# Performance work log

Measured on AMD Instinct MI355X. Metric: run time of the kernel, lower is better.

The kernel has to match this reference:

```python
import jax, jax.numpy as jnp
import numpy as np

D, N, M = 256, 8192, 8192
DISTANCE_THRESH = 0.8


def setup_inputs() -> dict:
    key = jax.random.key(0)
    k0, k1 = jax.random.split(key)
    d0 = jax.random.normal(k0, (D, N), dtype=jnp.float32)
    d1 = jax.random.normal(k1, (D, M), dtype=jnp.float32)
    # descriptors are L2-normalized along the feature dim (cosine similarity,
    # consistent with the 2*(1-sim) squared-distance formula in the module)
    d0 = d0 / jnp.linalg.norm(d0, axis=0, keepdims=True)
    d1 = d1 / jnp.linalg.norm(d1, axis=0, keepdims=True)
    return {"descriptors0": d0, "descriptors1": d1}


def reference(descriptors0, descriptors1):
    # nn_sim: [N, M] similarity matrix
    nn_sim = jnp.einsum('dn,dm->nm', descriptors0, descriptors1)
    nn_dist_01 = jnp.max(nn_sim, axis=1)          # [N]
    nn_idx_01 = jnp.argmax(nn_sim, axis=1)        # [N]
    nn_idx_10 = jnp.argmax(nn_sim, axis=0)        # [M]
    nn_dist = 2.0 * (1.0 - nn_dist_01)            # squared L2 dist for unit vecs
    ids1 = jnp.arange(nn_sim.shape[0])
    mask = ids1 == nn_idx_10[nn_idx_01]           # mutual NN check
    if DISTANCE_THRESH > 0.0:
        mask = mask & (nn_dist <= DISTANCE_THRESH ** 2)
    matches = jnp.where(mask, nn_idx_01, -1)
    scores = jnp.where(mask, (nn_dist + 1.0) / 2.0, 0.0)
    return matches, scores
```

## Files before the change

kernel.cpp:

```cpp
#include <hip/hip_runtime.h>
#include <hip/hip_bf16.h>

typedef __attribute__((ext_vector_type(8))) short short8;
typedef __attribute__((ext_vector_type(4))) float floatx4;
typedef unsigned int u32;

#define D_DIM 256
#define TCOLS 32
#define TILES 8
#define IDX_BITS 0x1FFFu
#define VAL_MASK 0xFFFFE000u


__device__ inline unsigned short f2bf_rne(float f) {
  u32 u = __float_as_uint(f);
  u32 r = (u + 0x7FFFu + ((u >> 16) & 1u)) >> 16;
  return (unsigned short)r;
}

__device__ inline u32 umax(u32 a, u32 b) { return a > b ? a : b; }


__global__ __launch_bounds__(256) void transpose_cast2(const float* __restrict__ d0,
                                                       const float* __restrict__ d1,
                                                       unsigned short* __restrict__ At,
                                                       unsigned short* __restrict__ Bt2,
                                                       int N, int M,
                                                       u32* __restrict__ best, int init_n) {
  __shared__ alignas(16) unsigned short tile[64 * 132];
  const int tid = threadIdx.x;
  const int bx = blockIdx.x;
  const int nblkA = N / 64;
  const bool isA = bx < nblkA;
  const float* src = isA ? d0 : d1;
  const int C = isA ? N : M;
  const int gd0 = (isA ? bx : bx - nblkA) * 64;
  const int d = tid & 63;
  const int fy = blockIdx.y;
#pragma unroll
  for (int k = 0; k < 32; ++k) {
    int fl = (tid >> 6) + 4 * k;
    float v = src[(size_t)(fy * 128 + fl) * C + gd0 + d];
    tile[d * 132 + fl] = f2bf_rne(v);
  }
  __syncthreads();
  if (isA) {
#pragma unroll
    for (int c = 0; c < 4; ++c) {
      int slot = c * 256 + tid;
      int dd = slot >> 4, f8 = slot & 15;
      short8 o = *(const short8*)(tile + dd * 132 + f8 * 8);
      *(short8*)(At + (size_t)(gd0 + dd) * D_DIM + fy * 128 + f8 * 8) = o;
    }
  } else {
#pragma unroll
    for (int c = 0; c < 4; ++c) {
      int slot = c * 256 + tid;
      int dd = slot & 63;
      int f8l = c * 4 + (tid >> 6);
      int f8g = fy * 16 + f8l;
      short8 o = *(const short8*)(tile + dd * 132 + f8l * 8);
      size_t off = (size_t)((gd0 + dd) >> 5) * 8192 + (size_t)(f8g >> 2) * 1024 +
                   (size_t)((dd >> 4) & 1) * 512 + (f8g & 3) * 128 + (dd & 15) * 8;
      *(short8*)(Bt2 + off) = o;
    }
  }
  if (fy == 0) {
    int i = bx * 256 + tid;
    if (i < init_n) best[i] = 0u;
  }
}

template <bool PRECAST>
__global__ __launch_bounds__(256, 2) void gemm_reduce(const float* __restrict__ A,
                                                      const unsigned short* __restrict__ At,
                                                      const unsigned short* __restrict__ Bt2,
                                                      u32* __restrict__ best01,
                                                      u32* __restrict__ best10,
                                                      int N, int M) {
  __shared__ u32 colbest[TILES * TCOLS];

  const int tid  = threadIdx.x;
  const int wave = tid >> 6;
  const int lane = tid & 63;
  const int quad = lane >> 4;
  const int l15  = lane & 15;

  const int xB = N >> 8, yB = M >> 8;
  const int bid = blockIdx.x;
  int x, y;
  if ((yB & 7) == 0) {
    int c = bid & 7, k = bid >> 3;
    x = k % xB;
    y = c * (yB >> 3) + k / xB;
  } else {
    x = bid % xB;
    y = bid / xB;
  }
  const int n0  = x * 256;
  const int mg0 = y * (TILES * TCOLS);
  const int rbase = n0 + wave * 64;

  colbest[tid] = 0u;

  short8 af[4][8];
  if constexpr (PRECAST) {
#pragma unroll
    for (int t = 0; t < 4; ++t) {
      const unsigned short* ap = At + (size_t)(rbase + t * 16 + l15) * D_DIM + quad * 8;
#pragma unroll
      for (int kc = 0; kc < 8; ++kc)
        af[t][kc] = *(const short8*)(ap + kc * 32);
    }
  } else {
#pragma unroll
    for (int t = 0; t < 4; ++t)
#pragma unroll
      for (int kc = 0; kc < 8; ++kc) {
        const int row = rbase + t * 16 + l15;
        const int kb = kc * 32 + quad * 8;
        short8 o;
#pragma unroll
        for (int u = 0; u < 8; ++u)
          o[u] = (short)f2bf_rne(A[(size_t)(kb + u) * N + row]);
        af[t][kc] = o;
      }
  }

  const unsigned short* bp = Bt2 + (size_t)(mg0 >> 5) * 8192 + (size_t)lane * 8;

  short8 bfA[4][2];
#pragma unroll
  for (int kc = 0; kc < 4; ++kc)
#pragma unroll
    for (int j = 0; j < 2; ++j)
      bfA[kc][j] = *(const short8*)(bp + (kc * 2 + j) * 512);

  u32 rbk[16];
#pragma unroll
  for (int s = 0; s < 16; ++s) rbk[s] = 0u;
  const u32 rp0 = 0x1FFFu - (u32)(rbase + quad * 4);

  __syncthreads();

  for (int mt = 0; mt < TILES; ++mt) {
    const unsigned short* bpt = bp + (size_t)mt * 8192;
    floatx4 acc[4][2];
#pragma unroll
    for (int i = 0; i < 4; ++i)
#pragma unroll
      for (int j = 0; j < 2; ++j)
        acc[i][j] = (floatx4){2.0f, 2.0f, 2.0f, 2.0f};

#pragma unroll
    for (int kc = 0; kc < 4; ++kc)
#pragma unroll
      for (int i = 0; i < 4; ++i)
#pragma unroll
        for (int j = 0; j < 2; ++j)
          acc[i][j] = __builtin_amdgcn_mfma_f32_16x16x32_bf16(af[i][kc], bfA[kc][j], acc[i][j], 0, 0, 0);

#pragma unroll
    for (int kc = 0; kc < 4; ++kc)
#pragma unroll
      for (int j = 0; j < 2; ++j)
        bfA[kc][j] = *(const short8*)(bpt + ((kc + 4) * 2 + j) * 512);

#pragma unroll
    for (int kc = 0; kc < 4; ++kc)
#pragma unroll
      for (int i = 0; i < 4; ++i)
#pragma unroll
        for (int j = 0; j < 2; ++j)
          acc[i][j] = __builtin_amdgcn_mfma_f32_16x16x32_bf16(af[i][kc + 4], bfA[kc][j], acc[i][j], 0, 0, 0);

    if (mt + 1 < TILES) {
#pragma unroll
      for (int kc = 0; kc < 4; ++kc)
#pragma unroll
        for (int j = 0; j < 2; ++j)
          bfA[kc][j] = *(const short8*)(bpt + 8192 + (kc * 2 + j) * 512);
    }

    const int m0 = mg0 + mt * TCOLS;
    u32 cb[2] = {0u, 0u};
    u32 colpay[2] = {0x1FFFu - (u32)(m0 + l15), 0x1FFFu - (u32)(m0 + 16 + l15)};
#pragma unroll
    for (int i = 0; i < 4; ++i)
#pragma unroll
      for (int r = 0; r < 4; ++r) {
        u32 rp = rp0 - (u32)(i * 16 + r);
        u32 rb = rbk[i * 4 + r];
#pragma unroll
        for (int j = 0; j < 2; ++j) {
          u32 u = __float_as_uint(acc[i][j][r]) & VAL_MASK;
          rb = umax(rb, u | colpay[j]);
          cb[j] = umax(cb[j], u | rp);
        }
        rbk[i * 4 + r] = rb;
      }
#pragma unroll
    for (int j = 0; j < 2; ++j) {
      u32 b = cb[j];
      b = umax(b, (u32)__shfl_xor((int)b, 16, 64));
      b = umax(b, (u32)__shfl_xor((int)b, 32, 64));
      if (quad == 0) atomicMax(&colbest[mt * TCOLS + j * 16 + l15], b);
    }
  }

#pragma unroll
  for (int i = 0; i < 4; ++i)
#pragma unroll
    for (int r = 0; r < 4; ++r) {
      u32 b = rbk[i * 4 + r];
      b = umax(b, (u32)__shfl_xor((int)b, 1, 64));
      b = umax(b, (u32)__shfl_xor((int)b, 2, 64));
      b = umax(b, (u32)__shfl_xor((int)b, 4, 64));
      b = umax(b, (u32)__shfl_xor((int)b, 8, 64));
      if (l15 == 0) atomicMax(&best01[rbase + i * 16 + quad * 4 + r], b);
    }

  __syncthreads();
  atomicMax(&best10[mg0 + tid], colbest[tid]);
}

__global__ void finalize(const u32* __restrict__ best01, const u32* __restrict__ best10,
                         float* __restrict__ out, int N) {
  int n = blockIdx.x * blockDim.x + threadIdx.x;
  if (n >= N) return;
  u32 k = best01[n];
  int idx01 = (int)((~k) & IDX_BITS);
  float sim = __uint_as_float(k & VAL_MASK) - 2.0f;
  int idx10 = (int)((~best10[idx01]) & IDX_BITS);
  float dist = 2.0f - 2.0f * sim;
  bool ok = (idx10 == n) && (dist <= 0.64f);
  out[n]     = ok ? (float)idx01 : -1.0f;
  out[N + n] = ok ? 1.5f - sim : 0.0f;
}


extern "C" void kernel_launch(void* const* d_in, const int* in_sizes, int n_in,
                              void* d_out, int out_size, void* d_ws, size_t ws_size,
                              hipStream_t stream) {
  (void)n_in; (void)out_size;
  const float* d0 = (const float*)d_in[0];
  const float* d1 = (const float*)d_in[1];
  const int N = in_sizes[0] / D_DIM;
  const int M = in_sizes[1] / D_DIM;

  u32* best01 = (u32*)d_ws;
  u32* best10 = best01 + N;
  unsigned short* At  = (unsigned short*)(best10 + M);
  unsigned short* Bt2 = At + (size_t)N * D_DIM;
  float* out = (float*)d_out;

  const int nBlocks = (N / 256) * (M / 256);
  const size_t need = (size_t)(N + M) * sizeof(u32) +
                      (size_t)(N + M) * D_DIM * sizeof(unsigned short);

  if (ws_size >= need) {
    hipLaunchKernelGGL(transpose_cast2, dim3((N + M) / 64, 2), dim3(256), 0, stream,
                       d0, d1, At, Bt2, N, M, best01, N + M);
    hipLaunchKernelGGL((gemm_reduce<true>), dim3(nBlocks), dim3(256), 0, stream,
                       d0, At, Bt2, best01, best10, N, M);
  } else {
    unsigned short* BtF = (unsigned short*)(best10 + M);
    hipLaunchKernelGGL(transpose_cast2, dim3(M / 64, 2), dim3(256), 0, stream,
                       d1, d1, BtF, BtF, 0, M, best01, N + M);
    hipLaunchKernelGGL((gemm_reduce<false>), dim3(nBlocks), dim3(256), 0, stream,
                       d0, BtF, BtF, best01, best10, N, M);
  }
  hipLaunchKernelGGL(finalize, dim3(N / 256), dim3(256), 0, stream, best01, best10, out, N);
}
```

Before: 114.3 us.

## Halve per-block row tile and drop B-fragment double buffering in GEMM-reduce

Shrinks each block's row tile from 256 to 128 (32 rows per wave), doubling the grid and halving the A-fragment registers per wave. The explicit software prefetch of B fragments across tiles is replaced by loading B inside the k-loop right before use, and the min-occupancy hint in launch bounds is removed. The intent is to lower register pressure and raise occupancy and grid parallelism. In exchange, each B fragment now feeds half as many MFMAs, global/L2 traffic for B doubles, and load latency is no longer explicitly hidden.

```diff
diff --git a/kernel.cpp b/kernel.cpp
--- a/kernel.cpp
+++ b/kernel.cpp
@@ -72,12 +72,12 @@
 }
 
 template <bool PRECAST>
-__global__ __launch_bounds__(256, 2) void gemm_reduce(const float* __restrict__ A,
-                                                      const unsigned short* __restrict__ At,
-                                                      const unsigned short* __restrict__ Bt2,
-                                                      u32* __restrict__ best01,
-                                                      u32* __restrict__ best10,
-                                                      int N, int M) {
+__global__ __launch_bounds__(256) void gemm_reduce(const float* __restrict__ A,
+                                                   const unsigned short* __restrict__ At,
+                                                   const unsigned short* __restrict__ Bt2,
+                                                   u32* __restrict__ best01,
+                                                   u32* __restrict__ best10,
+                                                   int N, int M) {
   __shared__ u32 colbest[TILES * TCOLS];
 
   const int tid  = threadIdx.x;
@@ -86,7 +86,7 @@
   const int quad = lane >> 4;
   const int l15  = lane & 15;
 
-  const int xB = N >> 8, yB = M >> 8;
+  const int xB = N >> 7, yB = M >> 8;
   const int bid = blockIdx.x;
   int x, y;
   if ((yB & 7) == 0) {
@@ -97,16 +97,16 @@
     x = bid % xB;
     y = bid / xB;
   }
-  const int n0  = x * 256;
+  const int n0  = x * 128;
   const int mg0 = y * (TILES * TCOLS);
-  const int rbase = n0 + wave * 64;
+  const int rbase = n0 + wave * 32;
 
   colbest[tid] = 0u;
 
-  short8 af[4][8];
+  short8 af[2][8];
   if constexpr (PRECAST) {
 #pragma unroll
-    for (int t = 0; t < 4; ++t) {
+    for (int t = 0; t < 2; ++t) {
       const unsigned short* ap = At + (size_t)(rbase + t * 16 + l15) * D_DIM + quad * 8;
 #pragma unroll
       for (int kc = 0; kc < 8; ++kc)
@@ -114,7 +114,7 @@
     }
   } else {
 #pragma unroll
-    for (int t = 0; t < 4; ++t)
+    for (int t = 0; t < 2; ++t)
 #pragma unroll
       for (int kc = 0; kc < 8; ++kc) {
         const int row = rbase + t * 16 + l15;
@@ -129,64 +129,37 @@
 
   const unsigned short* bp = Bt2 + (size_t)(mg0 >> 5) * 8192 + (size_t)lane * 8;
 
-  short8 bfA[4][2];
-#pragma unroll
-  for (int kc = 0; kc < 4; ++kc)
-#pragma unroll
-    for (int j = 0; j < 2; ++j)
-      bfA[kc][j] = *(const short8*)(bp + (kc * 2 + j) * 512);
-
-  u32 rbk[16];
-#pragma unroll
-  for (int s = 0; s < 16; ++s) rbk[s] = 0u;
+  u32 rbk[8];
+#pragma unroll
+  for (int s = 0; s < 8; ++s) rbk[s] = 0u;
   const u32 rp0 = 0x1FFFu - (u32)(rbase + quad * 4);
 
   __syncthreads();
 
   for (int mt = 0; mt < TILES; ++mt) {
     const unsigned short* bpt = bp + (size_t)mt * 8192;
-    floatx4 acc[4][2];
-#pragma unroll
-    for (int i = 0; i < 4; ++i)
+    floatx4 acc[2][2];
+#pragma unroll
+    for (int i = 0; i < 2; ++i)
 #pragma unroll
       for (int j = 0; j < 2; ++j)
         acc[i][j] = (floatx4){2.0f, 2.0f, 2.0f, 2.0f};
 
 #pragma unroll
-    for (int kc = 0; kc < 4; ++kc)
-#pragma unroll
-      for (int i = 0; i < 4; ++i)
-#pragma unroll
-        for (int j = 0; j < 2; ++j)
-          acc[i][j] = __builtin_amdgcn_mfma_f32_16x16x32_bf16(af[i][kc], bfA[kc][j], acc[i][j], 0, 0, 0);
-
-#pragma unroll
-    for (int kc = 0; kc < 4; ++kc)
-#pragma unroll
-      for (int j = 0; j < 2; ++j)
-        bfA[kc][j] = *(const short8*)(bpt + ((kc + 4) * 2 + j) * 512);
-
-#pragma unroll
-    for (int kc = 0; kc < 4; ++kc)
-#pragma unroll
-      for (int i = 0; i < 4; ++i)
-#pragma unroll
-        for (int j = 0; j < 2; ++j)
-          acc[i][j] = __builtin_amdgcn_mfma_f32_16x16x32_bf16(af[i][kc + 4], bfA[kc][j], acc[i][j], 0, 0, 0);
-
-    if (mt + 1 < TILES) {
-#pragma unroll
-      for (int kc = 0; kc < 4; ++kc)
-#pragma unroll
-        for (int j = 0; j < 2; ++j)
-          bfA[kc][j] = *(const short8*)(bpt + 8192 + (kc * 2 + j) * 512);
+    for (int kc = 0; kc < 8; ++kc) {
+      short8 bf0 = *(const short8*)(bpt + (kc * 2 + 0) * 512);
+      short8 bf1 = *(const short8*)(bpt + (kc * 2 + 1) * 512);
+      acc[0][0] = __builtin_amdgcn_mfma_f32_16x16x32_bf16(af[0][kc], bf0, acc[0][0], 0, 0, 0);
+      acc[1][0] = __builtin_amdgcn_mfma_f32_16x16x32_bf16(af[1][kc], bf0, acc[1][0], 0, 0, 0);
+      acc[0][1] = __builtin_amdgcn_mfma_f32_16x16x32_bf16(af[0][kc], bf1, acc[0][1], 0, 0, 0);
+      acc[1][1] = __builtin_amdgcn_mfma_f32_16x16x32_bf16(af[1][kc], bf1, acc[1][1], 0, 0, 0);
     }
 
     const int m0 = mg0 + mt * TCOLS;
     u32 cb[2] = {0u, 0u};
     u32 colpay[2] = {0x1FFFu - (u32)(m0 + l15), 0x1FFFu - (u32)(m0 + 16 + l15)};
 #pragma unroll
-    for (int i = 0; i < 4; ++i)
+    for (int i = 0; i < 2; ++i)
 #pragma unroll
       for (int r = 0; r < 4; ++r) {
         u32 rp = rp0 - (u32)(i * 16 + r);
@@ -209,7 +182,7 @@
   }
 
 #pragma unroll
-  for (int i = 0; i < 4; ++i)
+  for (int i = 0; i < 2; ++i)
 #pragma unroll
     for (int r = 0; r < 4; ++r) {
       u32 b = rbk[i * 4 + r];
@@ -254,7 +227,7 @@
   unsigned short* Bt2 = At + (size_t)N * D_DIM;
   float* out = (float*)d_out;
 
-  const int nBlocks = (N / 256) * (M / 256);
+  const int nBlocks = (N / 128) * (M / 256);
   const size_t need = (size_t)(N + M) * sizeof(u32) +
                       (size_t)(N + M) * D_DIM * sizeof(unsigned short);
 
```

After: 170.5 us. 49.2% more time.
